# Kernel tuning notes

Hardware: AMD Instinct MI355X
Metric: run time of the kernel (lower is better)

The kernel has to match this reference:

```python
import jax, jax.numpy as jnp
import numpy as np
import math

PHI = (1 + math.sqrt(5)) / 2
TABLE_SIZE = 4096
TWO_PI = 2.0 * math.pi
_ang = np.arange(TABLE_SIZE, dtype=np.float32) * (TWO_PI / TABLE_SIZE)
SIN_T = jnp.asarray(np.sin(_ang))
COS_T = jnp.asarray(np.cos(_ang))


def lookup_sin_cos(theta):
    """LUT sin/cos with linear interpolation over a 4096-entry table on [0, 2pi)."""
    pos = (theta / TWO_PI % 1.0) * TABLE_SIZE
    i0f = jnp.floor(pos)
    frac = pos - i0f
    i0 = i0f.astype(jnp.int32) % TABLE_SIZE
    i1 = (i0 + 1) % TABLE_SIZE
    s = SIN_T[i0] * (1.0 - frac) + SIN_T[i1] * frac
    c = COS_T[i0] * (1.0 - frac) + COS_T[i1] * frac
    return s, c


def setup_inputs() -> dict:
    key = jax.random.key(0)
    ks = jax.random.split(key, 8)
    B, S, D, H = 2, 2048, 1024, 16
    dh = D // H
    return {
        "x": jax.random.normal(ks[0], (B, S, D), dtype=jnp.float32),
        "w_q": jax.random.normal(ks[1], (H, dh), dtype=jnp.float32) * 0.02,
        "b_q": jnp.zeros((H, dh), jnp.float32),
        "phi_q": jnp.full((H, dh), PHI, jnp.float32),
        "w_k": jax.random.normal(ks[2], (H, dh), dtype=jnp.float32) * 0.02,
        "b_k": jnp.zeros((H, dh), jnp.float32),
        "phi_k": jnp.full((H, dh), PHI, jnp.float32),
        "w_v": jax.random.normal(ks[3], (H, dh), dtype=jnp.float32) * 0.02,
        "b_v": jnp.zeros((H, dh), jnp.float32),
        "w_out": jax.random.normal(ks[4], (D,), dtype=jnp.float32) * 0.02,
        "b_out": jnp.zeros((D,), jnp.float32),
    }


def reference(x, w_q, b_q, phi_q, w_k, b_k, phi_k, w_v, b_v, w_out, b_out):
    B, S, D = x.shape
    H, dh = w_q.shape
    scale = math.sqrt(2 * dh)
    t = jnp.arange(S, dtype=x.dtype).reshape(1, S, 1, 1)
    xh = x.reshape(B, S, H, dh)

    theta_q = xh / (1.0 + jnp.abs(w_q)) + b_q + t * phi_q
    sin_q, cos_q = lookup_sin_cos(theta_q)
    Q = jnp.concatenate([cos_q, sin_q], axis=-1)  # (B,S,H,2dh)

    theta_k = xh / (1.0 + jnp.abs(w_k)) + b_k + t * phi_k
    sin_k, cos_k = lookup_sin_cos(theta_k)
    K = jnp.concatenate([cos_k, sin_k], axis=-1)  # (B,S,H,2dh)

    theta_v = xh / (1.0 + jnp.abs(w_v)) + b_v
    sin_v, cos_v = lookup_sin_cos(theta_v)
    V = cos_v + sin_v  # (B,S,H,dh)

    scores = jnp.einsum('bqhd,bkhd->bhqk', Q, K) / scale
    causal = jnp.triu(jnp.ones((S, S), dtype=bool), k=1)
    scores = jnp.where(causal, -jnp.inf, scores)
    attn = jax.nn.softmax(scores, axis=-1)
    out = jnp.einsum('bhqk,bkhd->bqhd', attn, V).reshape(B, S, D)

    theta_out = out / (1.0 + jnp.abs(w_out)) + b_out
    sin_o, cos_o = lookup_sin_cos(theta_out)
    return cos_o + sin_o
```

## Files before the change

### kernel.cpp

```cpp
#include <hip/hip_runtime.h>
#include <hip/hip_bf16.h>
#include <math.h>

#define BB 2
#define SS 2048
#define HH 16
#define DH 64
#define DQK 128
#define DD (HH*DH)
#define QS2   0.12751758f
#define EBIAS 11.5415605f

typedef _Float16 half8_t __attribute__((ext_vector_type(8)));
typedef _Float16 half4_t __attribute__((ext_vector_type(4)));
typedef __fp16  fp16x2_t __attribute__((ext_vector_type(2)));
typedef float f32x4_t __attribute__((ext_vector_type(4)));
typedef float f32x4v __attribute__((ext_vector_type(4)));

__device__ __forceinline__ void fsincos(float th, float* sn, float* cs) {
  float rev = th * 0.15915494309189535f;
  rev -= floorf(rev);
  float ang = rev * 6.283185307179586f;
  *sn = __sinf(ang);
  *cs = __cosf(ang);
}

__device__ __forceinline__ void dma16(const void* g, void* l) {
  __builtin_amdgcn_global_load_lds(
      (const __attribute__((address_space(1))) unsigned int*)g,
      (__attribute__((address_space(3))) unsigned int*)l, 16, 0, 0);
}

__global__ __launch_bounds__(256) void gen_qkv(
    const float* __restrict__ x,
    const float* __restrict__ wq, const float* __restrict__ bq,
    const float* __restrict__ phq,
    const float* __restrict__ wk, const float* __restrict__ bk,
    const float* __restrict__ phk,
    const float* __restrict__ wv, const float* __restrict__ bv,
    _Float16* __restrict__ Qd, _Float16* __restrict__ Kd, _Float16* __restrict__ Vtd)
{
  int stile = blockIdx.x & 31;
  int bh    = blockIdx.x >> 5;
  int b = bh >> 4, h = bh & 15;
  int t = threadIdx.x;
  int sl = t >> 2;
  int dq = (t & 3) << 4;
  int s  = stile * 64 + sl;

  __shared__ _Float16 Vl[64 * 65];

  const float* xr = x + (((size_t)b * SS + s) * HH + h) * DH + dq;
  float xv[16];
#pragma unroll
  for (int i = 0; i < 4; i++)
    *(f32x4v*)(&xv[i * 4]) = *(const f32x4v*)(xr + i * 4);

  int hd0 = h * DH + dq;
  float iwqv[16], vbq[16], vpq[16];
  float iwkv[16], vbk[16], vpk[16];
  float iwvv[16], vbv[16];
#pragma unroll
  for (int i = 0; i < 4; i++) {
    f32x4v w4, b4, p4;
    w4 = *(const f32x4v*)(wq + hd0 + i * 4);
    b4 = *(const f32x4v*)(bq + hd0 + i * 4);
    p4 = *(const f32x4v*)(phq + hd0 + i * 4);
#pragma unroll
    for (int j = 0; j < 4; j++) {
      iwqv[i*4+j] = __builtin_amdgcn_rcpf(1.f + fabsf(w4[j]));
      vbq[i*4+j] = b4[j]; vpq[i*4+j] = p4[j];
    }
    w4 = *(const f32x4v*)(wk + hd0 + i * 4);
    b4 = *(const f32x4v*)(bk + hd0 + i * 4);
    p4 = *(const f32x4v*)(phk + hd0 + i * 4);
#pragma unroll
    for (int j = 0; j < 4; j++) {
      iwkv[i*4+j] = __builtin_amdgcn_rcpf(1.f + fabsf(w4[j]));
      vbk[i*4+j] = b4[j]; vpk[i*4+j] = p4[j];
    }
    w4 = *(const f32x4v*)(wv + hd0 + i * 4);
    b4 = *(const f32x4v*)(bv + hd0 + i * 4);
#pragma unroll
    for (int j = 0; j < 4; j++) {
      iwvv[i*4+j] = __builtin_amdgcn_rcpf(1.f + fabsf(w4[j]));
      vbv[i*4+j] = b4[j];
    }
  }

  float tv = (float)s;
  _Float16 qc[16], qs[16], kc[16], ks[16];
#pragma unroll
  for (int i = 0; i < 16; i++) {
    int d = dq + i;
    {
      float th = xv[i] * iwqv[i] + vbq[i] + tv * vpq[i];
      float sn, cs; fsincos(th, &sn, &cs);
      qc[i] = (_Float16)(cs * QS2);
      qs[i] = (_Float16)(sn * QS2);
    }
    {
      float th = xv[i] * iwkv[i] + vbk[i] + tv * vpk[i];
      float sn, cs; fsincos(th, &sn, &cs);
      kc[i] = (_Float16)cs;
      ks[i] = (_Float16)sn;
    }
    {
      float th = xv[i] * iwvv[i] + vbv[i];
      float sn, cs; fsincos(th, &sn, &cs);
      Vl[d * 65 + sl] = (_Float16)(cs + sn);
    }
  }
  size_t qbase = ((size_t)bh * SS + s) * DQK;
#pragma unroll
  for (int i = 0; i < 2; i++) {
    *(half8_t*)(Qd + qbase + dq + i * 8)      = *(half8_t*)(&qc[i * 8]);
    *(half8_t*)(Qd + qbase + DH + dq + i * 8) = *(half8_t*)(&qs[i * 8]);
  }
  {
    size_t ktb = ((size_t)bh * 32 + stile) * 8192;
    int fo0 = (t & 3) * 2;
    *(half8_t*)(Kd + ktb + ((size_t)(fo0    ) * 64 + sl) * 8) = *(half8_t*)(&kc[0]);
    *(half8_t*)(Kd + ktb + ((size_t)(fo0 + 1) * 64 + sl) * 8) = *(half8_t*)(&kc[8]);
    *(half8_t*)(Kd + ktb + ((size_t)(fo0 + 8) * 64 + sl) * 8) = *(half8_t*)(&ks[0]);
    *(half8_t*)(Kd + ktb + ((size_t)(fo0 + 9) * 64 + sl) * 8) = *(half8_t*)(&ks[8]);
  }
  __syncthreads();
#pragma unroll
  for (int i = 0; i < 2; i++) {
    int u = t * 2 + i;
    int dv = u & 63, ku = u >> 6;
    _Float16 tmp[8];
#pragma unroll
    for (int jj = 0; jj < 8; jj++) tmp[jj] = Vl[dv * 65 + ku * 8 + jj];
    *(half8_t*)(Vtd + (((size_t)bh * 32 + stile) * 8 + ku) * 512 + dv * 8) =
        *(half8_t*)tmp;
  }
}

__global__ __launch_bounds__(256, 4) void flash_attn(
    const _Float16* __restrict__ Qd, const _Float16* __restrict__ Kd,
    const _Float16* __restrict__ Vtd,
    const float* __restrict__ wout, const float* __restrict__ bout,
    float* __restrict__ out)
{
  int g  = blockIdx.x >> 5;
  int bh = blockIdx.x & 31;
  int r8 = g & 7, tier = g >> 3;
  int nch = (tier == 0) ? 32 - r8 : (tier == 1) ? 1 + r8
          : (tier == 2) ? 24 - r8 : 9 + r8;
  int qt = nch - 1;
  int b  = bh >> 4, hh = bh & 15;
  int q0 = qt * 64;
  int wave = threadIdx.x >> 6;
  int lane = threadIdx.x & 63;
  int lm = lane & 15, lq = lane >> 4;
  int qh = wave >> 1;
  int kh = wave & 1;

  __shared__ __align__(16) _Float16 KV[2][8192];

  const _Float16* Kg = Kd + (size_t)bh * 32 * 8192;
  const _Float16* Vg = Vtd + (size_t)bh * 32 * 4096;

  {
#pragma unroll
    for (int i = 0; i < 4; i++)
      dma16(Kg + (size_t)(wave * 4 + i) * 512 + lane * 8, &KV[0][(wave * 4 + i) * 512]);
  }

  const _Float16* Qb = Qd + ((size_t)bh * SS + q0 + qh * 32) * DQK;
  half8_t aq[2][4];
#pragma unroll
  for (int qtl = 0; qtl < 2; qtl++)
#pragma unroll
    for (int c = 0; c < 4; c++)
      aq[qtl][c] = *(const half8_t*)(Qb + (qtl * 16 + lm) * DQK + c * 32 + lq * 8);

  f32x4_t o[4][2];
  float l[2] = {0.f, 0.f};
#pragma unroll
  for (int dt = 0; dt < 4; dt++)
#pragma unroll
    for (int qtl = 0; qtl < 2; qtl++) o[dt][qtl] = (f32x4_t){0.f, 0.f, 0.f, 0.f};

  const f32x4_t cinit = (f32x4_t){-EBIAS, -EBIAS, -EBIAS, -EBIAS};

  const _Float16* vbase = Vg + ((size_t)(kh * 4 + (lq >> 1)) * 64 + lm) * 8 + (lq & 1) * 4;

  for (int kt = 0; kt < nch; ++kt) {
    int bf = kt & 1;
    __syncthreads();
    if (kt + 1 < nch) {
      int nb = (kt + 1) & 1;
      const _Float16* gK = Kg + (size_t)(kt + 1) * 8192;
#pragma unroll
      for (int i = 0; i < 4; i++)
        dma16(gK + (size_t)(wave * 4 + i) * 512 + lane * 8, &KV[nb][(wave * 4 + i) * 512]);
    }

    const _Float16* lK = &KV[bf][0];
    int k0 = kt * 64;

    f32x4_t cST[2][2];
    cST[0][0] = cST[0][1] = cST[1][0] = cST[1][1] = cinit;
    __builtin_amdgcn_s_setprio(1);
#pragma unroll
    for (int c = 0; c < 4; c++) {
      half8_t k0f = *(const half8_t*)(lK + ((size_t)(c * 4 + lq) * 64 + kh * 32 + lm) * 8);
      half8_t k1f = *(const half8_t*)(lK + ((size_t)(c * 4 + lq) * 64 + kh * 32 + 16 + lm) * 8);
      cST[0][0] = __builtin_amdgcn_mfma_f32_16x16x32_f16(k0f, aq[0][c], cST[0][0], 0, 0, 0);
      cST[0][1] = __builtin_amdgcn_mfma_f32_16x16x32_f16(k0f, aq[1][c], cST[0][1], 0, 0, 0);
      cST[1][0] = __builtin_amdgcn_mfma_f32_16x16x32_f16(k1f, aq[0][c], cST[1][0], 0, 0, 0);
      cST[1][1] = __builtin_amdgcn_mfma_f32_16x16x32_f16(k1f, aq[1][c], cST[1][1], 0, 0, 0);
    }
    __builtin_amdgcn_s_setprio(0);

    const _Float16* gV = vbase + (size_t)kt * 4096;
    half4_t vfr[4][2];
#pragma unroll
    for (int dt = 0; dt < 4; dt++)
#pragma unroll
      for (int kg = 0; kg < 2; kg++)
        vfr[dt][kg] = *(const half4_t*)(gV + kg * 1024 + dt * 128);

    bool maskit = (kt == nch - 1);
    half4_t pb[2][2];
#pragma unroll
    for (int ktl = 0; ktl < 2; ktl++)
#pragma unroll
      for (int qtl = 0; qtl < 2; qtl++) {
        float pf[4];
#pragma unroll
        for (int r = 0; r < 4; r++) {
          float sv = cST[ktl][qtl][r];
          if (maskit) {
            int key  = k0 + kh * 32 + ktl * 16 + lq * 4 + r;
            int qrow = q0 + qh * 32 + qtl * 16 + lm;
            if (key > qrow) sv = -1e30f;
          }
          pf[r] = __builtin_exp2f(sv);
          l[qtl] += pf[r];
        }
        fp16x2_t h01 = __builtin_amdgcn_cvt_pkrtz(pf[0], pf[1]);
        fp16x2_t h23 = __builtin_amdgcn_cvt_pkrtz(pf[2], pf[3]);
        pb[ktl][qtl] = (half4_t){(_Float16)h01.x, (_Float16)h01.y,
                                 (_Float16)h23.x, (_Float16)h23.y};
      }

    __builtin_amdgcn_s_setprio(1);
#pragma unroll
    for (int dt = 0; dt < 4; dt++)
#pragma unroll
      for (int kg = 0; kg < 2; kg++) {
        o[dt][0] = __builtin_amdgcn_mfma_f32_16x16x16f16(vfr[dt][kg], pb[kg][0], o[dt][0], 0, 0, 0);
        o[dt][1] = __builtin_amdgcn_mfma_f32_16x16x16f16(vfr[dt][kg], pb[kg][1], o[dt][1], 0, 0, 0);
      }
    __builtin_amdgcn_s_setprio(0);
  }

#pragma unroll
  for (int qtl = 0; qtl < 2; qtl++) {
    l[qtl] += __shfl_xor(l[qtl], 16);
    l[qtl] += __shfl_xor(l[qtl], 32);
  }

  float* Ot = (float*)&KV[0][0];
  float* Lf = Ot + 64 * 67;
  __syncthreads();
  if (kh == 1) {
#pragma unroll
    for (int qtl = 0; qtl < 2; qtl++) {
      int row = qh * 32 + qtl * 16 + lm;
#pragma unroll
      for (int dt = 0; dt < 4; dt++)
#pragma unroll
        for (int rr = 0; rr < 4; rr++)
          Ot[(dt * 16 + lq * 4 + rr) * 67 + row] = o[dt][qtl][rr];
      if (lq == 0) Lf[row] = l[qtl];
    }
  }
  __syncthreads();
  if (kh == 0) {
#pragma unroll
    for (int qtl = 0; qtl < 2; qtl++) {
      int row = qh * 32 + qtl * 16 + lm;
      float rl = __builtin_amdgcn_rcpf(l[qtl] + Lf[row]);
#pragma unroll
      for (int dt = 0; dt < 4; dt++)
#pragma unroll
        for (int rr = 0; rr < 4; rr++) {
          int idx = (dt * 16 + lq * 4 + rr) * 67 + row;
          Ot[idx] = (o[dt][qtl][rr] + Ot[idx]) * rl;
        }
    }
  }
  __syncthreads();
  {
    int dcol = hh * DH + lane;
    float iw = __builtin_amdgcn_rcpf(1.f + fabsf(wout[dcol]));
    float bo = bout[dcol];
#pragma unroll
    for (int rr = 0; rr < 16; rr++) {
      int row = wave * 16 + rr;
      float th = Ot[lane * 67 + row] * iw + bo;
      float sn, cs; fsincos(th, &sn, &cs);
      out[((size_t)b * SS + q0 + row) * DD + dcol] = cs + sn;
    }
  }
}

extern "C" void kernel_launch(void* const* d_in, const int* in_sizes, int n_in,
                              void* d_out, int out_size, void* d_ws, size_t ws_size,
                              hipStream_t stream) {
  (void)in_sizes; (void)n_in; (void)out_size; (void)ws_size;
  const float* x   = (const float*)d_in[0];
  const float* wq  = (const float*)d_in[1];
  const float* bq  = (const float*)d_in[2];
  const float* phq = (const float*)d_in[3];
  const float* wk  = (const float*)d_in[4];
  const float* bk  = (const float*)d_in[5];
  const float* phk = (const float*)d_in[6];
  const float* wv  = (const float*)d_in[7];
  const float* bv  = (const float*)d_in[8];
  const float* wo  = (const float*)d_in[9];
  const float* bo  = (const float*)d_in[10];

  _Float16* Qd  = (_Float16*)d_ws;
  _Float16* Kd  = Qd + (size_t)BB * HH * SS * DQK;
  _Float16* Vtd = Kd + (size_t)BB * HH * SS * DQK;

  gen_qkv<<<BB * HH * (SS / 64), 256, 0, stream>>>(
      x, wq, bq, phq, wk, bk, phk, wv, bv, Qd, Kd, Vtd);
  flash_attn<<<32 * 32, 256, 0, stream>>>(
      Qd, Kd, Vtd, wo, bo, (float*)d_out);
}
```

Before: 143.5 us.

## Persistent work-queue flash attention with split long q-tiles and LDS-staged V

Replaces the fixed one-block-per-tile grid with persistent blocks that pull work items from per-group atomic counters. A lookup table orders the items longest first. The longest query tiles (qt>=16) are split into two key-range halves, and their partial O and l are merged through global blobs using an atomic flag handshake. V is now DMA'd into LDS alongside K instead of being read straight from global memory, and the setprio hints and the 4-blocks occupancy bound are removed. The aim is better load balance across the causal triangle, at the cost of atomics, the blob round trip, and a larger LDS footprint.

```diff
diff --git a/kernel.cpp b/kernel.cpp
--- a/kernel.cpp
+++ b/kernel.cpp
@@ -138,174 +138,226 @@
   }
 }
 
-__global__ __launch_bounds__(256, 4) void flash_attn(
+__device__ const unsigned char kTab[48] = {
+  125,127,123, 60,121,117,119,115, 56,113,109,111,107, 52,105,101,
+  103, 99, 48, 97, 93, 95, 91, 44, 89, 85, 87, 83, 40, 81, 77, 79,
+   75, 36, 73, 69, 71, 67, 32, 65, 28, 24, 20, 16, 12,  8,  4,  0};
+
+__global__ __launch_bounds__(256) void flash_attn(
     const _Float16* __restrict__ Qd, const _Float16* __restrict__ Kd,
     const _Float16* __restrict__ Vtd,
     const float* __restrict__ wout, const float* __restrict__ bout,
-    float* __restrict__ out)
+    float* __restrict__ out,
+    unsigned* __restrict__ ctr, unsigned* __restrict__ flags,
+    float* __restrict__ blobs)
 {
-  int g  = blockIdx.x >> 5;
-  int bh = blockIdx.x & 31;
-  int r8 = g & 7, tier = g >> 3;
-  int nch = (tier == 0) ? 32 - r8 : (tier == 1) ? 1 + r8
-          : (tier == 2) ? 24 - r8 : 9 + r8;
-  int qt = nch - 1;
-  int b  = bh >> 4, hh = bh & 15;
-  int q0 = qt * 64;
+  int myq = blockIdx.x & 7;
   int wave = threadIdx.x >> 6;
   int lane = threadIdx.x & 63;
   int lm = lane & 15, lq = lane >> 4;
   int qh = wave >> 1;
   int kh = wave & 1;
 
-  __shared__ __align__(16) _Float16 KV[2][8192];
-
-  const _Float16* Kg = Kd + (size_t)bh * 32 * 8192;
-  const _Float16* Vg = Vtd + (size_t)bh * 32 * 4096;
-
-  {
-#pragma unroll
-    for (int i = 0; i < 4; i++)
-      dma16(Kg + (size_t)(wave * 4 + i) * 512 + lane * 8, &KV[0][(wave * 4 + i) * 512]);
-  }
-
-  const _Float16* Qb = Qd + ((size_t)bh * SS + q0 + qh * 32) * DQK;
-  half8_t aq[2][4];
-#pragma unroll
-  for (int qtl = 0; qtl < 2; qtl++)
-#pragma unroll
-    for (int c = 0; c < 4; c++)
-      aq[qtl][c] = *(const half8_t*)(Qb + (qtl * 16 + lm) * DQK + c * 32 + lq * 8);
-
-  f32x4_t o[4][2];
-  float l[2] = {0.f, 0.f};
-#pragma unroll
-  for (int dt = 0; dt < 4; dt++)
-#pragma unroll
-    for (int qtl = 0; qtl < 2; qtl++) o[dt][qtl] = (f32x4_t){0.f, 0.f, 0.f, 0.f};
-
-  const f32x4_t cinit = (f32x4_t){-EBIAS, -EBIAS, -EBIAS, -EBIAS};
-
-  const _Float16* vbase = Vg + ((size_t)(kh * 4 + (lq >> 1)) * 64 + lm) * 8 + (lq & 1) * 4;
-
-  for (int kt = 0; kt < nch; ++kt) {
-    int bf = kt & 1;
-    __syncthreads();
-    if (kt + 1 < nch) {
-      int nb = (kt + 1) & 1;
-      const _Float16* gK = Kg + (size_t)(kt + 1) * 8192;
+  __shared__ __align__(16) _Float16 KV[2][12288];
+  __shared__ int sItem;
+
+  for (;;) {
+    __syncthreads();
+    if (threadIdx.x == 0) {
+      int got = -1;
+      for (int a = 0; a < 8; a++) {
+        int qq = (myq + a) & 7;
+        unsigned v = atomicAdd(&ctr[qq], 1u);
+        if (v < 192u) { got = (qq << 8) | (int)v; break; }
+      }
+      sItem = got;
+    }
+    __syncthreads();
+    int it = sItem;
+    if (it < 0) break;
+    int qq = it >> 8, u = it & 255;
+    int bh = qq + 8 * (u & 3);
+    int code = kTab[u >> 2];
+    int st = code & 1, sp = (code >> 1) & 1, qt = code >> 2;
+    int nch = qt + 1, hhalf = nch >> 1;
+    int c0 = st ? (sp ? hhalf : 0) : 0;
+    int c1 = st ? (sp ? nch : hhalf) : nch;
+
+    int b = bh >> 4, hh = bh & 15;
+    int q0 = qt * 64;
+
+    const _Float16* Kg = Kd + (size_t)bh * 32 * 8192;
+    const _Float16* Vg = Vtd + (size_t)bh * 32 * 4096;
+
+    {
+      const _Float16* gK = Kg + (size_t)c0 * 8192;
+      const _Float16* gV = Vg + (size_t)c0 * 4096;
+      int nb = c0 & 1;
 #pragma unroll
       for (int i = 0; i < 4; i++)
         dma16(gK + (size_t)(wave * 4 + i) * 512 + lane * 8, &KV[nb][(wave * 4 + i) * 512]);
-    }
-
-    const _Float16* lK = &KV[bf][0];
-    int k0 = kt * 64;
-
-    f32x4_t cST[2][2];
-    cST[0][0] = cST[0][1] = cST[1][0] = cST[1][1] = cinit;
-    __builtin_amdgcn_s_setprio(1);
-#pragma unroll
-    for (int c = 0; c < 4; c++) {
-      half8_t k0f = *(const half8_t*)(lK + ((size_t)(c * 4 + lq) * 64 + kh * 32 + lm) * 8);
-      half8_t k1f = *(const half8_t*)(lK + ((size_t)(c * 4 + lq) * 64 + kh * 32 + 16 + lm) * 8);
-      cST[0][0] = __builtin_amdgcn_mfma_f32_16x16x32_f16(k0f, aq[0][c], cST[0][0], 0, 0, 0);
-      cST[0][1] = __builtin_amdgcn_mfma_f32_16x16x32_f16(k0f, aq[1][c], cST[0][1], 0, 0, 0);
-      cST[1][0] = __builtin_amdgcn_mfma_f32_16x16x32_f16(k1f, aq[0][c], cST[1][0], 0, 0, 0);
-      cST[1][1] = __builtin_amdgcn_mfma_f32_16x16x32_f16(k1f, aq[1][c], cST[1][1], 0, 0, 0);
-    }
-    __builtin_amdgcn_s_setprio(0);
-
-    const _Float16* gV = vbase + (size_t)kt * 4096;
-    half4_t vfr[4][2];
+#pragma unroll
+      for (int i = 0; i < 2; i++)
+        dma16(gV + (size_t)(wave * 2 + i) * 512 + lane * 8, &KV[nb][8192 + (wave * 2 + i) * 512]);
+    }
+
+    const _Float16* Qb = Qd + ((size_t)bh * SS + q0 + qh * 32) * DQK;
+    half8_t aq[2][4];
+#pragma unroll
+    for (int qtl = 0; qtl < 2; qtl++)
+#pragma unroll
+      for (int c = 0; c < 4; c++)
+        aq[qtl][c] = *(const half8_t*)(Qb + (qtl * 16 + lm) * DQK + c * 32 + lq * 8);
+
+    f32x4_t o[4][2];
+    float l[2] = {0.f, 0.f};
 #pragma unroll
     for (int dt = 0; dt < 4; dt++)
 #pragma unroll
-      for (int kg = 0; kg < 2; kg++)
-        vfr[dt][kg] = *(const half4_t*)(gV + kg * 1024 + dt * 128);
-
-    bool maskit = (kt == nch - 1);
-    half4_t pb[2][2];
-#pragma unroll
-    for (int ktl = 0; ktl < 2; ktl++)
+      for (int qtl = 0; qtl < 2; qtl++) o[dt][qtl] = (f32x4_t){0.f, 0.f, 0.f, 0.f};
+
+    const f32x4_t cinit = (f32x4_t){-EBIAS, -EBIAS, -EBIAS, -EBIAS};
+
+    for (int kt = c0; kt < c1; ++kt) {
+      int bf = kt & 1;
+      __syncthreads();
+      if (kt + 1 < c1) {
+        int nb = (kt + 1) & 1;
+        const _Float16* gK = Kg + (size_t)(kt + 1) * 8192;
+        const _Float16* gV = Vg + (size_t)(kt + 1) * 4096;
+#pragma unroll
+        for (int i = 0; i < 4; i++)
+          dma16(gK + (size_t)(wave * 4 + i) * 512 + lane * 8, &KV[nb][(wave * 4 + i) * 512]);
+#pragma unroll
+        for (int i = 0; i < 2; i++)
+          dma16(gV + (size_t)(wave * 2 + i) * 512 + lane * 8, &KV[nb][8192 + (wave * 2 + i) * 512]);
+      }
+
+      const _Float16* lK = &KV[bf][0];
+      const _Float16* lV = &KV[bf][8192];
+      int k0 = kt * 64;
+
+      f32x4_t cST[2][2];
+      cST[0][0] = cST[0][1] = cST[1][0] = cST[1][1] = cinit;
+#pragma unroll
+      for (int c = 0; c < 4; c++) {
+        half8_t k0f = *(const half8_t*)(lK + ((size_t)(c * 4 + lq) * 64 + kh * 32 + lm) * 8);
+        half8_t k1f = *(const half8_t*)(lK + ((size_t)(c * 4 + lq) * 64 + kh * 32 + 16 + lm) * 8);
+        cST[0][0] = __builtin_amdgcn_mfma_f32_16x16x32_f16(k0f, aq[0][c], cST[0][0], 0, 0, 0);
+        cST[0][1] = __builtin_amdgcn_mfma_f32_16x16x32_f16(k0f, aq[1][c], cST[0][1], 0, 0, 0);
+        cST[1][0] = __builtin_amdgcn_mfma_f32_16x16x32_f16(k1f, aq[0][c], cST[1][0], 0, 0, 0);
+        cST[1][1] = __builtin_amdgcn_mfma_f32_16x16x32_f16(k1f, aq[1][c], cST[1][1], 0, 0, 0);
+      }
+
+      bool maskit = (kt == nch - 1);
+      half4_t pb[2][2];
+#pragma unroll
+      for (int ktl = 0; ktl < 2; ktl++)
+#pragma unroll
+        for (int qtl = 0; qtl < 2; qtl++) {
+          float pf[4];
+#pragma unroll
+          for (int r = 0; r < 4; r++) {
+            float sv = cST[ktl][qtl][r];
+            if (maskit) {
+              int key  = k0 + kh * 32 + ktl * 16 + lq * 4 + r;
+              int qrow = q0 + qh * 32 + qtl * 16 + lm;
+              if (key > qrow) sv = -1e30f;
+            }
+            pf[r] = __builtin_exp2f(sv);
+            l[qtl] += pf[r];
+          }
+          fp16x2_t h01 = __builtin_amdgcn_cvt_pkrtz(pf[0], pf[1]);
+          fp16x2_t h23 = __builtin_amdgcn_cvt_pkrtz(pf[2], pf[3]);
+          pb[ktl][qtl] = (half4_t){(_Float16)h01.x, (_Float16)h01.y,
+                                   (_Float16)h23.x, (_Float16)h23.y};
+        }
+
+#pragma unroll
+      for (int dt = 0; dt < 4; dt++)
+#pragma unroll
+        for (int kg = 0; kg < 2; kg++) {
+          half4_t vf = *(const half4_t*)(lV +
+              ((size_t)(kh * 4 + kg * 2 + (lq >> 1)) * 64 + dt * 16 + lm) * 8 + (lq & 1) * 4);
+          o[dt][0] = __builtin_amdgcn_mfma_f32_16x16x16f16(vf, pb[kg][0], o[dt][0], 0, 0, 0);
+          o[dt][1] = __builtin_amdgcn_mfma_f32_16x16x16f16(vf, pb[kg][1], o[dt][1], 0, 0, 0);
+        }
+    }
+
+#pragma unroll
+    for (int qtl = 0; qtl < 2; qtl++) {
+      l[qtl] += __shfl_xor(l[qtl], 16);
+      l[qtl] += __shfl_xor(l[qtl], 32);
+    }
+
+    if (st) {
+      int pair = bh * 16 + (qt - 16);
+      float* myb = blobs + ((size_t)(pair * 2 + sp) * 256 + threadIdx.x) * 36;
+#pragma unroll
+      for (int dt = 0; dt < 4; dt++)
+#pragma unroll
+        for (int qtl = 0; qtl < 2; qtl++)
+          *(f32x4_t*)(myb + (dt * 2 + qtl) * 4) = o[dt][qtl];
+      myb[32] = l[0]; myb[33] = l[1];
+      __threadfence();
+      __syncthreads();
+      if (threadIdx.x == 0) sItem = (int)atomicAdd(&flags[pair], 1u);
+      __syncthreads();
+      if (sItem == 0) continue;
+      __threadfence();
+      const float* ob = blobs + ((size_t)(pair * 2 + (sp ^ 1)) * 256 + threadIdx.x) * 36;
+#pragma unroll
+      for (int dt = 0; dt < 4; dt++)
+#pragma unroll
+        for (int qtl = 0; qtl < 2; qtl++) {
+          f32x4_t p = *(const f32x4_t*)(ob + (dt * 2 + qtl) * 4);
+          o[dt][qtl] += p;
+        }
+      l[0] += ob[32]; l[1] += ob[33];
+    }
+
+    float* Of = (float*)&KV[0][0];
+    float* Lf = Of + 64 * 68;
+    __syncthreads();
+    if (kh == 1) {
 #pragma unroll
       for (int qtl = 0; qtl < 2; qtl++) {
-        float pf[4];
-#pragma unroll
-        for (int r = 0; r < 4; r++) {
-          float sv = cST[ktl][qtl][r];
-          if (maskit) {
-            int key  = k0 + kh * 32 + ktl * 16 + lq * 4 + r;
-            int qrow = q0 + qh * 32 + qtl * 16 + lm;
-            if (key > qrow) sv = -1e30f;
+        int row = qh * 32 + qtl * 16 + lm;
+#pragma unroll
+        for (int dt = 0; dt < 4; dt++)
+#pragma unroll
+          for (int rr = 0; rr < 4; rr++)
+            Of[row * 68 + dt * 16 + lq * 4 + rr] = o[dt][qtl][rr];
+        if (lq == 0) Lf[row] = l[qtl];
+      }
+    }
+    __syncthreads();
+    if (kh == 0) {
+#pragma unroll
+      for (int qtl = 0; qtl < 2; qtl++) {
+        int row = qh * 32 + qtl * 16 + lm;
+        float rl = __builtin_amdgcn_rcpf(l[qtl] + Lf[row]);
+#pragma unroll
+        for (int dt = 0; dt < 4; dt++)
+#pragma unroll
+          for (int rr = 0; rr < 4; rr++) {
+            int idx = row * 68 + dt * 16 + lq * 4 + rr;
+            Of[idx] = (o[dt][qtl][rr] + Of[idx]) * rl;
           }
-          pf[r] = __builtin_exp2f(sv);
-          l[qtl] += pf[r];
-        }
-        fp16x2_t h01 = __builtin_amdgcn_cvt_pkrtz(pf[0], pf[1]);
-        fp16x2_t h23 = __builtin_amdgcn_cvt_pkrtz(pf[2], pf[3]);
-        pb[ktl][qtl] = (half4_t){(_Float16)h01.x, (_Float16)h01.y,
-                                 (_Float16)h23.x, (_Float16)h23.y};
-      }
-
-    __builtin_amdgcn_s_setprio(1);
-#pragma unroll
-    for (int dt = 0; dt < 4; dt++)
-#pragma unroll
-      for (int kg = 0; kg < 2; kg++) {
-        o[dt][0] = __builtin_amdgcn_mfma_f32_16x16x16f16(vfr[dt][kg], pb[kg][0], o[dt][0], 0, 0, 0);
-        o[dt][1] = __builtin_amdgcn_mfma_f32_16x16x16f16(vfr[dt][kg], pb[kg][1], o[dt][1], 0, 0, 0);
-      }
-    __builtin_amdgcn_s_setprio(0);
-  }
-
-#pragma unroll
-  for (int qtl = 0; qtl < 2; qtl++) {
-    l[qtl] += __shfl_xor(l[qtl], 16);
-    l[qtl] += __shfl_xor(l[qtl], 32);
-  }
-
-  float* Ot = (float*)&KV[0][0];
-  float* Lf = Ot + 64 * 67;
-  __syncthreads();
-  if (kh == 1) {
-#pragma unroll
-    for (int qtl = 0; qtl < 2; qtl++) {
-      int row = qh * 32 + qtl * 16 + lm;
-#pragma unroll
-      for (int dt = 0; dt < 4; dt++)
-#pragma unroll
-        for (int rr = 0; rr < 4; rr++)
-          Ot[(dt * 16 + lq * 4 + rr) * 67 + row] = o[dt][qtl][rr];
-      if (lq == 0) Lf[row] = l[qtl];
-    }
-  }
-  __syncthreads();
-  if (kh == 0) {
-#pragma unroll
-    for (int qtl = 0; qtl < 2; qtl++) {
-      int row = qh * 32 + qtl * 16 + lm;
-      float rl = __builtin_amdgcn_rcpf(l[qtl] + Lf[row]);
-#pragma unroll
-      for (int dt = 0; dt < 4; dt++)
-#pragma unroll
-        for (int rr = 0; rr < 4; rr++) {
-          int idx = (dt * 16 + lq * 4 + rr) * 67 + row;
-          Ot[idx] = (o[dt][qtl][rr] + Ot[idx]) * rl;
-        }
-    }
-  }
-  __syncthreads();
-  {
-    int dcol = hh * DH + lane;
-    float iw = __builtin_amdgcn_rcpf(1.f + fabsf(wout[dcol]));
-    float bo = bout[dcol];
-#pragma unroll
-    for (int rr = 0; rr < 16; rr++) {
-      int row = wave * 16 + rr;
-      float th = Ot[lane * 67 + row] * iw + bo;
-      float sn, cs; fsincos(th, &sn, &cs);
-      out[((size_t)b * SS + q0 + row) * DD + dcol] = cs + sn;
+      }
+    }
+    __syncthreads();
+    {
+      int dcol = hh * DH + lane;
+      float iw = __builtin_amdgcn_rcpf(1.f + fabsf(wout[dcol]));
+      float bo = bout[dcol];
+#pragma unroll
+      for (int rr = 0; rr < 16; rr++) {
+        int row = wave * 16 + rr;
+        float th = Of[row * 68 + lane] * iw + bo;
+        float sn, cs; fsincos(th, &sn, &cs);
+        out[((size_t)b * SS + q0 + row) * DD + dcol] = cs + sn;
+      }
     }
   }
 }
@@ -329,9 +381,14 @@
   _Float16* Qd  = (_Float16*)d_ws;
   _Float16* Kd  = Qd + (size_t)BB * HH * SS * DQK;
   _Float16* Vtd = Kd + (size_t)BB * HH * SS * DQK;
-
+  char* ctl = (char*)(Vtd + (size_t)BB * HH * SS * DH);
+  unsigned* ctr   = (unsigned*)ctl;
+  unsigned* flags = ctr + 8;
+  float* blobs = (float*)(ctl + 4096);
+
+  hipMemsetAsync(ctl, 0, (8 + 512) * 4, stream);
   gen_qkv<<<BB * HH * (SS / 64), 256, 0, stream>>>(
       x, wq, bq, phq, wk, bk, phk, wv, bv, Qd, Kd, Vtd);
-  flash_attn<<<32 * 32, 256, 0, stream>>>(
-      Qd, Kd, Vtd, wo, bo, (float*)d_out);
-}
+  flash_attn<<<768, 256, 0, stream>>>(
+      Qd, Kd, Vtd, wo, bo, (float*)d_out, ctr, flags, blobs);
+}
```

After: 415.6 us. 2.9x slower.

## Triple-buffer K and V tiles in LDS with vmcnt-based async pipeline

Applied to the files above, without the earlier changes.

The flash attention kernel now stages both K and V tiles into a 3-deep LDS ring using async DMA, issuing two tiles ahead and waiting with explicit vmcnt counts instead of a full __syncthreads per iteration. V fragments, which were loaded straight from global memory each iteration, are now read from LDS. It also drops the tiered block ordering in favour of a simple longest-first ordering, removes the setprio hints and the occupancy hint in launch_bounds, and changes the epilogue LDS layout to row-major with padding 68. LDS use grows to about 72KB per block, which may lower occupancy, and the hand-counted vmcnt values depend on the exact number of DMA instructions per stage.

```diff
diff --git a/kernel.cpp b/kernel.cpp
--- a/kernel.cpp
+++ b/kernel.cpp
@@ -138,19 +138,16 @@
   }
 }
 
-__global__ __launch_bounds__(256, 4) void flash_attn(
+__global__ __launch_bounds__(256) void flash_attn(
     const _Float16* __restrict__ Qd, const _Float16* __restrict__ Kd,
     const _Float16* __restrict__ Vtd,
     const float* __restrict__ wout, const float* __restrict__ bout,
     float* __restrict__ out)
 {
-  int g  = blockIdx.x >> 5;
+  int qt = 31 - (blockIdx.x >> 5);
   int bh = blockIdx.x & 31;
-  int r8 = g & 7, tier = g >> 3;
-  int nch = (tier == 0) ? 32 - r8 : (tier == 1) ? 1 + r8
-          : (tier == 2) ? 24 - r8 : 9 + r8;
-  int qt = nch - 1;
   int b  = bh >> 4, hh = bh & 15;
+  int nch = qt + 1;
   int q0 = qt * 64;
   int wave = threadIdx.x >> 6;
   int lane = threadIdx.x & 63;
@@ -158,17 +155,11 @@
   int qh = wave >> 1;
   int kh = wave & 1;
 
-  __shared__ __align__(16) _Float16 KV[2][8192];
+  __shared__ __align__(16) _Float16 KV[3][12288];
 
   const _Float16* Kg = Kd + (size_t)bh * 32 * 8192;
   const _Float16* Vg = Vtd + (size_t)bh * 32 * 4096;
 
-  {
-#pragma unroll
-    for (int i = 0; i < 4; i++)
-      dma16(Kg + (size_t)(wave * 4 + i) * 512 + lane * 8, &KV[0][(wave * 4 + i) * 512]);
-  }
-
   const _Float16* Qb = Qd + ((size_t)bh * SS + q0 + qh * 32) * DQK;
   half8_t aq[2][4];
 #pragma unroll
@@ -176,6 +167,22 @@
 #pragma unroll
     for (int c = 0; c < 4; c++)
       aq[qtl][c] = *(const half8_t*)(Qb + (qtl * 16 + lm) * DQK + c * 32 + lq * 8);
+  asm volatile("" ::: "memory");
+
+  auto STAGE = [&](int c) {
+    int rb = c % 3;
+    const _Float16* gK = Kg + (size_t)c * 8192;
+    const _Float16* gV = Vg + (size_t)c * 4096;
+#pragma unroll
+    for (int i = 0; i < 4; i++)
+      dma16(gK + (size_t)(wave * 4 + i) * 512 + lane * 8, &KV[rb][(wave * 4 + i) * 512]);
+#pragma unroll
+    for (int i = 0; i < 2; i++)
+      dma16(gV + (size_t)(wave * 2 + i) * 512 + lane * 8, &KV[rb][8192 + (wave * 2 + i) * 512]);
+  };
+
+  STAGE(0);
+  if (nch > 1) STAGE(1);
 
   f32x4_t o[4][2];
   float l[2] = {0.f, 0.f};
@@ -186,25 +193,20 @@
 
   const f32x4_t cinit = (f32x4_t){-EBIAS, -EBIAS, -EBIAS, -EBIAS};
 
-  const _Float16* vbase = Vg + ((size_t)(kh * 4 + (lq >> 1)) * 64 + lm) * 8 + (lq & 1) * 4;
-
   for (int kt = 0; kt < nch; ++kt) {
-    int bf = kt & 1;
-    __syncthreads();
-    if (kt + 1 < nch) {
-      int nb = (kt + 1) & 1;
-      const _Float16* gK = Kg + (size_t)(kt + 1) * 8192;
-#pragma unroll
-      for (int i = 0; i < 4; i++)
-        dma16(gK + (size_t)(wave * 4 + i) * 512 + lane * 8, &KV[nb][(wave * 4 + i) * 512]);
-    }
-
-    const _Float16* lK = &KV[bf][0];
+    if (kt + 1 < nch) asm volatile("s_waitcnt vmcnt(6)" ::: "memory");
+    else              asm volatile("s_waitcnt vmcnt(0)" ::: "memory");
+    __builtin_amdgcn_s_barrier();
+    asm volatile("" ::: "memory");
+    if (kt + 2 < nch) STAGE(kt + 2);
+
+    int rb = kt % 3;
+    const _Float16* lK = &KV[rb][0];
+    const _Float16* lV = &KV[rb][8192];
     int k0 = kt * 64;
 
     f32x4_t cST[2][2];
     cST[0][0] = cST[0][1] = cST[1][0] = cST[1][1] = cinit;
-    __builtin_amdgcn_s_setprio(1);
 #pragma unroll
     for (int c = 0; c < 4; c++) {
       half8_t k0f = *(const half8_t*)(lK + ((size_t)(c * 4 + lq) * 64 + kh * 32 + lm) * 8);
@@ -214,15 +216,6 @@
       cST[1][0] = __builtin_amdgcn_mfma_f32_16x16x32_f16(k1f, aq[0][c], cST[1][0], 0, 0, 0);
       cST[1][1] = __builtin_amdgcn_mfma_f32_16x16x32_f16(k1f, aq[1][c], cST[1][1], 0, 0, 0);
     }
-    __builtin_amdgcn_s_setprio(0);
-
-    const _Float16* gV = vbase + (size_t)kt * 4096;
-    half4_t vfr[4][2];
-#pragma unroll
-    for (int dt = 0; dt < 4; dt++)
-#pragma unroll
-      for (int kg = 0; kg < 2; kg++)
-        vfr[dt][kg] = *(const half4_t*)(gV + kg * 1024 + dt * 128);
 
     bool maskit = (kt == nch - 1);
     half4_t pb[2][2];
@@ -248,15 +241,15 @@
                                  (_Float16)h23.x, (_Float16)h23.y};
       }
 
-    __builtin_amdgcn_s_setprio(1);
 #pragma unroll
     for (int dt = 0; dt < 4; dt++)
 #pragma unroll
       for (int kg = 0; kg < 2; kg++) {
-        o[dt][0] = __builtin_amdgcn_mfma_f32_16x16x16f16(vfr[dt][kg], pb[kg][0], o[dt][0], 0, 0, 0);
-        o[dt][1] = __builtin_amdgcn_mfma_f32_16x16x16f16(vfr[dt][kg], pb[kg][1], o[dt][1], 0, 0, 0);
+        half4_t vf = *(const half4_t*)(lV +
+            ((size_t)(kh * 4 + kg * 2 + (lq >> 1)) * 64 + dt * 16 + lm) * 8 + (lq & 1) * 4);
+        o[dt][0] = __builtin_amdgcn_mfma_f32_16x16x16f16(vf, pb[kg][0], o[dt][0], 0, 0, 0);
+        o[dt][1] = __builtin_amdgcn_mfma_f32_16x16x16f16(vf, pb[kg][1], o[dt][1], 0, 0, 0);
       }
-    __builtin_amdgcn_s_setprio(0);
   }
 
 #pragma unroll
@@ -265,8 +258,8 @@
     l[qtl] += __shfl_xor(l[qtl], 32);
   }
 
-  float* Ot = (float*)&KV[0][0];
-  float* Lf = Ot + 64 * 67;
+  float* Of = (float*)&KV[0][0];
+  float* Lf = Of + 64 * 68;
   __syncthreads();
   if (kh == 1) {
 #pragma unroll
@@ -276,7 +269,7 @@
       for (int dt = 0; dt < 4; dt++)
 #pragma unroll
         for (int rr = 0; rr < 4; rr++)
-          Ot[(dt * 16 + lq * 4 + rr) * 67 + row] = o[dt][qtl][rr];
+          Of[row * 68 + dt * 16 + lq * 4 + rr] = o[dt][qtl][rr];
       if (lq == 0) Lf[row] = l[qtl];
     }
   }
@@ -290,8 +283,8 @@
       for (int dt = 0; dt < 4; dt++)
 #pragma unroll
         for (int rr = 0; rr < 4; rr++) {
-          int idx = (dt * 16 + lq * 4 + rr) * 67 + row;
-          Ot[idx] = (o[dt][qtl][rr] + Ot[idx]) * rl;
+          int idx = row * 68 + dt * 16 + lq * 4 + rr;
+          Of[idx] = (o[dt][qtl][rr] + Of[idx]) * rl;
         }
     }
   }
@@ -303,7 +296,7 @@
 #pragma unroll
     for (int rr = 0; rr < 16; rr++) {
       int row = wave * 16 + rr;
-      float th = Ot[lane * 67 + row] * iw + bo;
+      float th = Of[row * 68 + lane] * iw + bo;
       float sn, cs; fsincos(th, &sn, &cs);
       out[((size_t)b * SS + q0 + row) * DD + dcol] = cs + sn;
     }
```

Measured after the change: 147.8 us. 1.03x slower.
